# Performance work log

Hardware: AMD Instinct MI355X
Metric: run time of the kernel (lower is better)

The kernel has to match this reference:

```python
import jax, jax.numpy as jnp
import numpy as np

B, P, G, C = 64, 5000, 300, 20   # images, preds/img, gt/img, num classes
INPUT_SIZE = 512.0
IOU_THRESH = 0.5


def setup_inputs() -> dict:
    key = jax.random.key(0)
    k1, k2, k3, k4, k5, k6, k7 = jax.random.split(key, 7)
    # predictions: [x1,y1,x2,y2,score,cls], boxes normalized to [0,1]
    pxy = jax.random.uniform(k1, (B, P, 2), minval=0.0, maxval=0.8)
    pwh = jax.random.uniform(k2, (B, P, 2), minval=0.02, maxval=0.2)
    score = jax.random.uniform(k3, (B, P, 1))
    pcls = jax.random.randint(k4, (B, P, 1), 0, C).astype(jnp.float32)
    output = jnp.concatenate([pxy, pxy + pwh, score, pcls], axis=-1)
    # ground truth: [x1,y1,x2,y2,cls]
    txy = jax.random.uniform(k5, (B, G, 2), minval=0.0, maxval=0.8)
    twh = jax.random.uniform(k6, (B, G, 2), minval=0.02, maxval=0.2)
    tcls = jax.random.randint(k7, (B, G, 1), 0, C).astype(jnp.float32)
    labels = jnp.concatenate([txy, txy + twh, tcls], axis=-1)
    return {"output": output, "labels": labels}


def reference(output, labels):
    scale = jnp.array([INPUT_SIZE, INPUT_SIZE, INPUT_SIZE, INPUT_SIZE], dtype=output.dtype)

    def match_image(preds, targets):  # preds [P,6], targets [G,5]
        tcls = targets[:, 4]
        tboxes = targets[:, :4] * scale                     # [G,4]
        tarea = (tboxes[:, 2] - tboxes[:, 0]) * (tboxes[:, 3] - tboxes[:, 1])

        def step(detected, pred):
            pbox = pred[:4] * scale
            lt = jnp.maximum(pbox[:2], tboxes[:, :2])       # [G,2]
            rb = jnp.minimum(pbox[2:], tboxes[:, 2:])
            wh = jnp.clip(rb - lt, 0.0)
            inter = wh[:, 0] * wh[:, 1]
            parea = (pbox[2] - pbox[0]) * (pbox[3] - pbox[1])
            ious = inter / (parea + tarea - inter)          # [G]
            cls_mask = tcls == pred[5]
            masked = jnp.where(cls_mask, ious, -1.0)
            bi = jnp.argmax(masked)                          # greedy argmax over same-class gt
            match = ((pred[4] > 0)
                     & jnp.any(cls_mask)
                     & (masked[bi] > IOU_THRESH)
                     & (~detected[bi]))                      # sequential dedup
            detected = detected.at[bi].set(detected[bi] | match)
            return detected, match

        _, correct = jax.lax.scan(step, jnp.zeros(tboxes.shape[0], dtype=bool), preds)
        return correct                                       # [P] bool

    correct = jax.vmap(match_image)(output, labels).astype(output.dtype)  # [B,P]
    # stats: (correct flag, score, predicted class) per prediction; tcls per image
    stats = jnp.stack([correct, output[:, :, 4], output[:, :, 5]], axis=-1)  # [B,P,3]
    tcls = labels[:, :, 4]                                                    # [B,G]
    return stats, tcls
```

## Files before the change

### kernel.cpp

```cpp
#include <hip/hip_runtime.h>
#include <cstdint>

#define B 64
#define P 5000
#define G 300
#define C 20
#define SCALE_F 512.0f
#define IOU_TH 0.5f
#define NSPLIT 4
#define PCHUNK ((P + NSPLIT - 1) / NSPLIT)
#define NTA 512
#define SPT ((PCHUNK + NTA - 1) / NTA)
#define SENT 0x7FFFFFFF

#pragma clang fp contract(off)

__global__ __launch_bounds__(NTA) void match_kernel(
    const float* __restrict__ preds,
    const float* __restrict__ labels,
    int* __restrict__ blockfp,
    short* __restrict__ gbest)
{
    const int s = blockIdx.x;
    const int b = blockIdx.y;
    const int tid = threadIdx.x;

    __shared__ float4 sb[G];
    __shared__ float  sa[G];
    __shared__ short  ssi[G];
    __shared__ short  cls_s[G];
    __shared__ int    so[C + 1];
    __shared__ int    cnt[C];
    __shared__ int    pcnt[C];
    __shared__ int    firstp[G];
    __shared__ unsigned short psorted[PCHUNK];

    const float* lab = labels + (size_t)b * G * 5;
    const float* prd = preds + (size_t)b * P * 6;
    const int pbase = s * PCHUNK;

    if (tid < C) { cnt[tid] = 0; pcnt[tid] = 0; }
    for (int t = tid; t < G; t += NTA) {
        cls_s[t] = (short)(int)lab[t * 5 + 4];
        firstp[t] = SENT;
    }
    __syncthreads();

    for (int t = tid; t < G; t += NTA) atomicAdd(&cnt[cls_s[t]], 1);
    #pragma unroll
    for (int k = 0; k < SPT; ++k) {
        int p = pbase + k * NTA + tid;
        if (p < pbase + PCHUNK)
            atomicAdd(&pcnt[(int)prd[p * 6 + 5]], 1);
    }
    __syncthreads();

    if (tid == 0) {
        int a = 0;
        for (int c = 0; c < C; ++c) { so[c] = a; a += cnt[c]; }
        so[C] = a;
    }
    if (tid == 64) {
        int a = 0;
        for (int c = 0; c < C; ++c) { int v = pcnt[c]; pcnt[c] = a; a += v; }
    }
    __syncthreads();

    for (int t = tid; t < G; t += NTA) {
        short c = cls_s[t];
        int rank = 0;
        for (int u = 0; u < t; ++u) rank += (cls_s[u] == c) ? 1 : 0;
        int pos = so[c] + rank;
        float x1 = lab[t * 5 + 0] * SCALE_F;
        float y1 = lab[t * 5 + 1] * SCALE_F;
        float x2 = lab[t * 5 + 2] * SCALE_F;
        float y2 = lab[t * 5 + 3] * SCALE_F;
        sb[pos] = make_float4(x1, y1, x2, y2);
        sa[pos] = (x2 - x1) * (y2 - y1);
        ssi[pos] = (short)t;
    }
    #pragma unroll
    for (int k = 0; k < SPT; ++k) {
        int p = pbase + k * NTA + tid;
        if (p < pbase + PCHUNK) {
            int c = (int)prd[p * 6 + 5];
            int pos = atomicAdd(&pcnt[c], 1);
            psorted[pos] = (unsigned short)p;
        }
    }
    __syncthreads();

    #pragma unroll
    for (int k = 0; k < SPT; ++k) {
        int slot = k * NTA + tid;
        if (slot >= PCHUNK) continue;
        int p = psorted[slot];
        const float* pr = prd + p * 6;
        float px1 = pr[0] * SCALE_F;
        float py1 = pr[1] * SCALE_F;
        float px2 = pr[2] * SCALE_F;
        float py2 = pr[3] * SCALE_F;
        float score = pr[4];
        int c = (int)pr[5];
        float parea = (px2 - px1) * (py2 - py1);

        int lo = so[c], hi = so[c + 1];
        float best = -1.0f;
        int bi = -1;
        for (int j = lo; j < hi; ++j) {
            float4 tb = sb[j];
            float lx = fmaxf(px1, tb.x);
            float ly = fmaxf(py1, tb.y);
            float rx = fminf(px2, tb.z);
            float ry = fminf(py2, tb.w);
            float w = fmaxf(rx - lx, 0.0f);
            float h = fmaxf(ry - ly, 0.0f);
            float inter = w * h;
            float uni = (parea + sa[j]) - inter;
            float iou = inter / uni;
            if (iou > best) { best = iou; bi = ssi[j]; }
        }

        bool eligible = (score > 0.0f) && (hi > lo) && (best > IOU_TH);
        gbest[(size_t)b * P + p] = eligible ? (short)bi : (short)-1;
        if (eligible) atomicMin(&firstp[bi], p);
    }
    __syncthreads();

    for (int t = tid; t < G; t += NTA)
        blockfp[((size_t)b * NSPLIT + s) * G + t] = firstp[t];
}

__global__ __launch_bounds__(1024) void resolve_kernel(
    const float* __restrict__ preds,
    const float* __restrict__ labels,
    const int* __restrict__ blockfp,
    const short* __restrict__ gbest,
    float* __restrict__ out_stats,
    float* __restrict__ out_tcls)
{
    const int s = blockIdx.x;
    const int b = blockIdx.y;
    const int tid = threadIdx.x;

    __shared__ int lf[G];

    if (tid < G) {
        const int* fp = blockfp + (size_t)b * NSPLIT * G + tid;
        int m = fp[0];
        m = min(m, fp[G]);
        m = min(m, fp[2 * G]);
        m = min(m, fp[3 * G]);
        lf[tid] = m;
        if (s == 0) out_tcls[b * G + tid] = labels[((size_t)b * G + tid) * 5 + 4];
    }
    __syncthreads();

    const int pbase = s * PCHUNK;
    #pragma unroll
    for (int k = 0; k < 2; ++k) {
        int p = pbase + k * 1024 + tid;
        if (p >= pbase + PCHUNK) continue;
        size_t ip = (size_t)b * P + p;
        int bi = gbest[ip];
        float corr = (bi >= 0 && lf[bi] == p) ? 1.0f : 0.0f;
        out_stats[ip * 3 + 0] = corr;
        out_stats[ip * 3 + 1] = preds[ip * 6 + 4];
        out_stats[ip * 3 + 2] = preds[ip * 6 + 5];
    }
}

extern "C" void kernel_launch(void* const* d_in, const int* in_sizes, int n_in,
                              void* d_out, int out_size, void* d_ws, size_t ws_size,
                              hipStream_t stream) {
    const float* output = (const float*)d_in[0];
    const float* labels = (const float*)d_in[1];

    float* out_stats = (float*)d_out;
    float* out_tcls  = (float*)d_out + (size_t)B * P * 3;

    int* blockfp = (int*)d_ws;
    short* gbest = (short*)(blockfp + (size_t)B * NSPLIT * G);

    dim3 grid(NSPLIT, B);
    match_kernel<<<grid, NTA, 0, stream>>>(output, labels, blockfp, gbest);
    resolve_kernel<<<grid, 1024, 0, stream>>>(output, labels, blockfp, gbest,
                                              out_stats, out_tcls);
}
```

Measured before the change: 76.35 us.

## Write stats in match kernel and scatter matches from per-gt first-pred

```diff
diff --git a/kernel.cpp b/kernel.cpp
--- a/kernel.cpp
+++ b/kernel.cpp
@@ -7,7 +7,7 @@
 #define C 20
 #define SCALE_F 512.0f
 #define IOU_TH 0.5f
-#define NSPLIT 4
+#define NSPLIT 8
 #define PCHUNK ((P + NSPLIT - 1) / NSPLIT)
 #define NTA 512
 #define SPT ((PCHUNK + NTA - 1) / NTA)
@@ -15,11 +15,12 @@
 
 #pragma clang fp contract(off)
 
-__global__ __launch_bounds__(NTA) void match_kernel(
+__global__ __launch_bounds__(NTA, 4) void match_kernel(
     const float* __restrict__ preds,
     const float* __restrict__ labels,
     int* __restrict__ blockfp,
-    short* __restrict__ gbest)
+    float* __restrict__ out_stats,
+    float* __restrict__ out_tcls)
 {
     const int s = blockIdx.x;
     const int b = blockIdx.y;
@@ -41,8 +42,10 @@
 
     if (tid < C) { cnt[tid] = 0; pcnt[tid] = 0; }
     for (int t = tid; t < G; t += NTA) {
-        cls_s[t] = (short)(int)lab[t * 5 + 4];
+        float cf = lab[t * 5 + 4];
+        cls_s[t] = (short)(int)cf;
         firstp[t] = SENT;
+        if (s == 0) out_tcls[(size_t)b * G + t] = cf;
     }
     __syncthreads();
 
@@ -101,7 +104,8 @@
         float px2 = pr[2] * SCALE_F;
         float py2 = pr[3] * SCALE_F;
         float score = pr[4];
-        int c = (int)pr[5];
+        float clsf = pr[5];
+        int c = (int)clsf;
         float parea = (px2 - px1) * (py2 - py1);
 
         int lo = so[c], hi = so[c + 1];
@@ -122,8 +126,12 @@
         }
 
         bool eligible = (score > 0.0f) && (hi > lo) && (best > IOU_TH);
-        gbest[(size_t)b * P + p] = eligible ? (short)bi : (short)-1;
         if (eligible) atomicMin(&firstp[bi], p);
+
+        size_t ip3 = ((size_t)b * P + p) * 3;
+        out_stats[ip3 + 0] = 0.0f;
+        out_stats[ip3 + 1] = score;
+        out_stats[ip3 + 2] = clsf;
     }
     __syncthreads();
 
@@ -131,43 +139,21 @@
         blockfp[((size_t)b * NSPLIT + s) * G + t] = firstp[t];
 }
 
-__global__ __launch_bounds__(1024) void resolve_kernel(
-    const float* __restrict__ preds,
-    const float* __restrict__ labels,
+__global__ __launch_bounds__(320) void resolve_kernel(
     const int* __restrict__ blockfp,
-    const short* __restrict__ gbest,
-    float* __restrict__ out_stats,
-    float* __restrict__ out_tcls)
+    float* __restrict__ out_stats)
 {
-    const int s = blockIdx.x;
-    const int b = blockIdx.y;
-    const int tid = threadIdx.x;
+    const int b = blockIdx.x;
+    const int t = threadIdx.x;
+    if (t >= G) return;
 
-    __shared__ int lf[G];
+    const int* fp = blockfp + (size_t)b * NSPLIT * G + t;
+    int m = fp[0];
+    #pragma unroll
+    for (int s = 1; s < NSPLIT; ++s) m = min(m, fp[s * G]);
 
-    if (tid < G) {
-        const int* fp = blockfp + (size_t)b * NSPLIT * G + tid;
-        int m = fp[0];
-        m = min(m, fp[G]);
-        m = min(m, fp[2 * G]);
-        m = min(m, fp[3 * G]);
-        lf[tid] = m;
-        if (s == 0) out_tcls[b * G + tid] = labels[((size_t)b * G + tid) * 5 + 4];
-    }
-    __syncthreads();
-
-    const int pbase = s * PCHUNK;
-    #pragma unroll
-    for (int k = 0; k < 2; ++k) {
-        int p = pbase + k * 1024 + tid;
-        if (p >= pbase + PCHUNK) continue;
-        size_t ip = (size_t)b * P + p;
-        int bi = gbest[ip];
-        float corr = (bi >= 0 && lf[bi] == p) ? 1.0f : 0.0f;
-        out_stats[ip * 3 + 0] = corr;
-        out_stats[ip * 3 + 1] = preds[ip * 6 + 4];
-        out_stats[ip * 3 + 2] = preds[ip * 6 + 5];
-    }
+    if (m != SENT)
+        out_stats[((size_t)b * P + m) * 3] = 1.0f;
 }
 
 extern "C" void kernel_launch(void* const* d_in, const int* in_sizes, int n_in,
@@ -180,10 +166,9 @@
     float* out_tcls  = (float*)d_out + (size_t)B * P * 3;
 
     int* blockfp = (int*)d_ws;
-    short* gbest = (short*)(blockfp + (size_t)B * NSPLIT * G);
 
     dim3 grid(NSPLIT, B);
-    match_kernel<<<grid, NTA, 0, stream>>>(output, labels, blockfp, gbest);
-    resolve_kernel<<<grid, 1024, 0, stream>>>(output, labels, blockfp, gbest,
-                                              out_stats, out_tcls);
+    match_kernel<<<grid, NTA, 0, stream>>>(output, labels, blockfp,
+                                           out_stats, out_tcls);
+    resolve_kernel<<<dim3(B), 320, 0, stream>>>(blockfp, out_stats);
 }
```

New measurement: 73.35 us. 3.9% less time.
